# Kernel optimization log

Hardware: AMD Instinct MI355X
Metric: run time of the kernel (lower is better)

Reference implementation:

```python
import jax, jax.numpy as jnp
import numpy as np

SPARSITY = 0.9  # fraction of zeros in the weight matrix


def setup_inputs() -> dict:
    key = jax.random.key(0)
    k_x, k_w, k_m, k_b = jax.random.split(key, 4)
    in_features, out_features = 4096, 4096
    n_tokens = 8192
    x = jax.random.normal(k_x, (n_tokens, in_features), dtype=jnp.float32)
    weight = jax.random.normal(k_w, (out_features, in_features), dtype=jnp.float32)
    mask = jax.random.uniform(k_m, (out_features, in_features)) >= SPARSITY
    bias = jax.random.normal(k_b, (out_features,), dtype=jnp.float32)
    return {"x": x, "weight": weight, "mask": mask, "bias": bias}


def reference(x, weight, mask, bias):
    # SparseLinear.forward: batch_addmm(weight_sparse, x, bias) == x @ W^T + b
    # The sparse CSR/COO weight is represented here as (dense values * mask).
    w = jnp.where(mask, weight, jnp.zeros((), dtype=weight.dtype))
    return jnp.einsum('ni,oi->no', x, w) + bias
```

## Files before the change

kernel.cpp:

```cpp
#include <hip/hip_runtime.h>
#include <hip/hip_bf16.h>
#include <stdint.h>


#define MDIM 8192
#define NDIM 4096
#define KDIM 4096

typedef __bf16   bf16x8 __attribute__((ext_vector_type(8)));
typedef float    f32x4  __attribute__((ext_vector_type(4)));
typedef uint16_t u16x8  __attribute__((ext_vector_type(8)));

__device__ __forceinline__ uint16_t f32_to_bf16_rne(float f) {
  union { float f; uint32_t u; } v; v.f = f;
  uint32_t u = v.u;
  return (uint16_t)((u + 0x7fffu + ((u >> 16) & 1u)) >> 16);
}

__global__ void detect_mask_kernel(const uint32_t* __restrict__ mask,
                                   int* __restrict__ flag) {
  __shared__ int any_nonbool;
  if (threadIdx.x == 0) any_nonbool = 0;
  __syncthreads();
  int bad = 0;
  for (int i = threadIdx.x; i < 4096; i += 256) {
    uint32_t w = mask[i];
    bad |= (w > 1u) ? 1 : 0;
  }
  if (bad) any_nonbool = 1;
  __syncthreads();
  if (threadIdx.x == 0) *flag = any_nonbool;
}


__global__ void cvt_x_kernel(const float* __restrict__ x,
                             uint16_t* __restrict__ xh, int n8) {
  int i = blockIdx.x * blockDim.x + threadIdx.x;
  if (i >= n8) return;
  const float4* src = (const float4*)x + (size_t)i * 2;
  float4 a = src[0], b = src[1];
  u16x8 o;
  o[0] = f32_to_bf16_rne(a.x); o[1] = f32_to_bf16_rne(a.y);
  o[2] = f32_to_bf16_rne(a.z); o[3] = f32_to_bf16_rne(a.w);
  o[4] = f32_to_bf16_rne(b.x); o[5] = f32_to_bf16_rne(b.y);
  o[6] = f32_to_bf16_rne(b.z); o[7] = f32_to_bf16_rne(b.w);
  *((u16x8*)xh + i) = o;
}

__global__ void cvt_w_kernel(const float* __restrict__ w,
                             const void* __restrict__ mask,
                             const int* __restrict__ flag,
                             uint16_t* __restrict__ wh, int n8) {
  int i = blockIdx.x * blockDim.x + threadIdx.x;
  if (i >= n8) return;
  const float4* src = (const float4*)w + (size_t)i * 2;
  float4 a = src[0], b = src[1];
  float vals[8] = {a.x, a.y, a.z, a.w, b.x, b.y, b.z, b.w};
  int m[8];
  if (*flag) {
    uint64_t mb = *((const uint64_t*)mask + i);
#pragma unroll
    for (int j = 0; j < 8; ++j) m[j] = (int)((mb >> (8 * j)) & 0xffu);
  } else {
    const int4* mp = (const int4*)mask + (size_t)i * 2;
    int4 ma = mp[0], mb4 = mp[1];
    m[0] = ma.x; m[1] = ma.y; m[2] = ma.z; m[3] = ma.w;
    m[4] = mb4.x; m[5] = mb4.y; m[6] = mb4.z; m[7] = mb4.w;
  }
  u16x8 o;
#pragma unroll
  for (int j = 0; j < 8; ++j)
    o[j] = m[j] ? f32_to_bf16_rne(vals[j]) : (uint16_t)0;
  *((u16x8*)wh + i) = o;
}


__global__ __launch_bounds__(256) void gemm_bias_kernel(
    const uint16_t* __restrict__ A, const uint16_t* __restrict__ B,
    const float* __restrict__ bias, float* __restrict__ C) {
  constexpr int BM = 128, BN = 128, BK = 64;
  constexpr int NBN = NDIM / BN;
  constexpr int ROWB = BK * 2;

  __shared__ __align__(16) uint8_t smem[2 * BM * BK * 2];
  uint8_t* smA = smem;
  uint8_t* smB = smem + BM * BK * 2;

  const int bid = blockIdx.x;
  const int cpx = gridDim.x >> 3;
  const int wg  = (bid & 7) * cpx + (bid >> 3);
  const int bm  = wg / NBN;
  const int bn  = wg % NBN;

  const int tid  = threadIdx.x;
  const int wave = tid >> 6;
  const int lane = tid & 63;
  const int wm = wave >> 1, wn = wave & 1;
  const int fr = lane & 15;
  const int fq = lane >> 4;

  const int trow = tid >> 3;
  const int tcb  = (tid & 7) << 4;
  const int tcol = (tcb ^ ((trow & 7) << 4)) >> 1;

  const uint16_t* Ablk = A + (size_t)bm * BM * KDIM;
  const uint16_t* Bblk = B + (size_t)bn * BN * KDIM;

  const int swz = (lane & 7) << 4;
  const int rdA = (wm * 64 + fr) * ROWB;
  const int rdB = (wn * 64 + fr) * ROWB;
  const int cb0 = fq * 16;

  f32x4 acc[4][4] = {};

  for (int k0 = 0; k0 < KDIM; k0 += BK) {
#pragma unroll
    for (int is = 0; is < 4; ++is) {
      const uint16_t* src = Ablk + (size_t)(is * 32 + trow) * KDIM + (k0 + tcol);
      __builtin_amdgcn_global_load_lds(
          (const __attribute__((address_space(1))) void*)src,
          (__attribute__((address_space(3))) void*)(smA + is * 4096 + wave * 1024),
          16, 0, 0);
    }
#pragma unroll
    for (int is = 0; is < 4; ++is) {
      const uint16_t* src = Bblk + (size_t)(is * 32 + trow) * KDIM + (k0 + tcol);
      __builtin_amdgcn_global_load_lds(
          (const __attribute__((address_space(1))) void*)src,
          (__attribute__((address_space(3))) void*)(smB + is * 4096 + wave * 1024),
          16, 0, 0);
    }
    __syncthreads();

#pragma unroll
    for (int ks = 0; ks < 2; ++ks) {
      const int cb = cb0 + ks * 64;
      bf16x8 af[4], bfr[4];
#pragma unroll
      for (int mi = 0; mi < 4; ++mi)
        af[mi] = *(const bf16x8*)(smA + rdA + mi * 16 * ROWB + (cb ^ swz));
#pragma unroll
      for (int ni = 0; ni < 4; ++ni)
        bfr[ni] = *(const bf16x8*)(smB + rdB + ni * 16 * ROWB + (cb ^ swz));
#pragma unroll
      for (int mi = 0; mi < 4; ++mi)
#pragma unroll
        for (int ni = 0; ni < 4; ++ni)
          acc[mi][ni] = __builtin_amdgcn_mfma_f32_16x16x32_bf16(
              af[mi], bfr[ni], acc[mi][ni], 0, 0, 0);
    }
    __syncthreads();
  }

  const int rowg0 = bm * BM + wm * 64 + fq * 4;
  const int colg0 = bn * BN + wn * 64 + fr;
#pragma unroll
  for (int ni = 0; ni < 4; ++ni) {
    const int col = colg0 + ni * 16;
    const float bv = bias[col];
#pragma unroll
    for (int mi = 0; mi < 4; ++mi) {
#pragma unroll
      for (int j = 0; j < 4; ++j) {
        const int row = rowg0 + mi * 16 + j;
        C[(size_t)row * NDIM + col] = acc[mi][ni][j] + bv;
      }
    }
  }
}

extern "C" void kernel_launch(void* const* d_in, const int* in_sizes, int n_in,
                              void* d_out, int out_size, void* d_ws, size_t ws_size,
                              hipStream_t stream) {
  const float* x    = (const float*)d_in[0];
  const float* w    = (const float*)d_in[1];
  const void*  mk   = (const void*)d_in[2];
  const float* bias = (const float*)d_in[3];
  float* out        = (float*)d_out;

  const size_t need = (size_t)MDIM * KDIM * 2 + (size_t)NDIM * KDIM * 2;
  if (ws_size < need) return;

  uint16_t* xh = (uint16_t*)d_ws;
  uint16_t* wh = xh + (size_t)MDIM * KDIM;

  int* flag = (int*)d_out;
  detect_mask_kernel<<<1, 256, 0, stream>>>((const uint32_t*)mk, flag);

  const int nx8 = MDIM * KDIM / 8;
  const int nw8 = NDIM * KDIM / 8;
  cvt_x_kernel<<<nx8 / 256, 256, 0, stream>>>(x, xh, nx8);
  cvt_w_kernel<<<nw8 / 256, 256, 0, stream>>>(w, mk, flag, wh, nw8);

  const int grid = (MDIM / 128) * (NDIM / 128);
  gemm_bias_kernel<<<grid, 256, 0, stream>>>(xh, wh, bias, out);
}
```

Before: 680.3 us.

## Use 256x256 GEMM tiles with double-buffered async LDS loads and grid-stride converts

Moves the bf16 GEMM from 128x128 tiles with 4 waves to 256x256 tiles with 8 waves. Each wave now computes a 128x64 sub-tile, which raises data reuse per LDS byte. Global-to-LDS loads are double-buffered two tiles ahead, using partial vmcnt waits and raw barriers so loads overlap the MFMA work, and s_setprio is raised around the MFMA bursts. The conversion kernels switch to grid-stride loops with a fixed grid of 2048 blocks. The cost is more registers (128 accumulator floats per thread), 128 KB of LDS per block, and only 512 blocks in the grid, which may hurt occupancy or tail balance.

```diff
diff --git a/kernel.cpp b/kernel.cpp
--- a/kernel.cpp
+++ b/kernel.cpp
@@ -32,134 +32,164 @@
   if (threadIdx.x == 0) *flag = any_nonbool;
 }
 
-
 __global__ void cvt_x_kernel(const float* __restrict__ x,
                              uint16_t* __restrict__ xh, int n8) {
-  int i = blockIdx.x * blockDim.x + threadIdx.x;
-  if (i >= n8) return;
-  const float4* src = (const float4*)x + (size_t)i * 2;
-  float4 a = src[0], b = src[1];
-  u16x8 o;
-  o[0] = f32_to_bf16_rne(a.x); o[1] = f32_to_bf16_rne(a.y);
-  o[2] = f32_to_bf16_rne(a.z); o[3] = f32_to_bf16_rne(a.w);
-  o[4] = f32_to_bf16_rne(b.x); o[5] = f32_to_bf16_rne(b.y);
-  o[6] = f32_to_bf16_rne(b.z); o[7] = f32_to_bf16_rne(b.w);
-  *((u16x8*)xh + i) = o;
+  const int stride = gridDim.x * blockDim.x;
+  for (int i = blockIdx.x * blockDim.x + threadIdx.x; i < n8; i += stride) {
+    const float4* src = (const float4*)x + (size_t)i * 2;
+    float4 a = src[0], b = src[1];
+    u16x8 o;
+    o[0] = f32_to_bf16_rne(a.x); o[1] = f32_to_bf16_rne(a.y);
+    o[2] = f32_to_bf16_rne(a.z); o[3] = f32_to_bf16_rne(a.w);
+    o[4] = f32_to_bf16_rne(b.x); o[5] = f32_to_bf16_rne(b.y);
+    o[6] = f32_to_bf16_rne(b.z); o[7] = f32_to_bf16_rne(b.w);
+    *((u16x8*)xh + i) = o;
+  }
 }
 
 __global__ void cvt_w_kernel(const float* __restrict__ w,
                              const void* __restrict__ mask,
                              const int* __restrict__ flag,
                              uint16_t* __restrict__ wh, int n8) {
-  int i = blockIdx.x * blockDim.x + threadIdx.x;
-  if (i >= n8) return;
-  const float4* src = (const float4*)w + (size_t)i * 2;
-  float4 a = src[0], b = src[1];
-  float vals[8] = {a.x, a.y, a.z, a.w, b.x, b.y, b.z, b.w};
-  int m[8];
-  if (*flag) {
-    uint64_t mb = *((const uint64_t*)mask + i);
-#pragma unroll
-    for (int j = 0; j < 8; ++j) m[j] = (int)((mb >> (8 * j)) & 0xffu);
-  } else {
-    const int4* mp = (const int4*)mask + (size_t)i * 2;
-    int4 ma = mp[0], mb4 = mp[1];
-    m[0] = ma.x; m[1] = ma.y; m[2] = ma.z; m[3] = ma.w;
-    m[4] = mb4.x; m[5] = mb4.y; m[6] = mb4.z; m[7] = mb4.w;
-  }
-  u16x8 o;
-#pragma unroll
-  for (int j = 0; j < 8; ++j)
-    o[j] = m[j] ? f32_to_bf16_rne(vals[j]) : (uint16_t)0;
-  *((u16x8*)wh + i) = o;
-}
-
-
-__global__ __launch_bounds__(256) void gemm_bias_kernel(
+  const int stride = gridDim.x * blockDim.x;
+  const int isU8 = *flag;
+  for (int i = blockIdx.x * blockDim.x + threadIdx.x; i < n8; i += stride) {
+    const float4* src = (const float4*)w + (size_t)i * 2;
+    float4 a = src[0], b = src[1];
+    float vals[8] = {a.x, a.y, a.z, a.w, b.x, b.y, b.z, b.w};
+    int m[8];
+    if (isU8) {
+      uint64_t mb = *((const uint64_t*)mask + i);
+#pragma unroll
+      for (int j = 0; j < 8; ++j) m[j] = (int)((mb >> (8 * j)) & 0xffu);
+    } else {
+      const int4* mp = (const int4*)mask + (size_t)i * 2;
+      int4 ma = mp[0], mb4 = mp[1];
+      m[0] = ma.x; m[1] = ma.y; m[2] = ma.z; m[3] = ma.w;
+      m[4] = mb4.x; m[5] = mb4.y; m[6] = mb4.z; m[7] = mb4.w;
+    }
+    u16x8 o;
+#pragma unroll
+    for (int j = 0; j < 8; ++j)
+      o[j] = m[j] ? f32_to_bf16_rne(vals[j]) : (uint16_t)0;
+    *((u16x8*)wh + i) = o;
+  }
+}
+
+
+#define BARRIER() do { asm volatile("" ::: "memory");            \
+                       __builtin_amdgcn_s_barrier();             \
+                       asm volatile("" ::: "memory"); } while (0)
+#define WAITV8()  asm volatile("s_waitcnt vmcnt(8)" ::: "memory")
+#define WAITV0()  asm volatile("s_waitcnt vmcnt(0)" ::: "memory")
+
+__global__ __launch_bounds__(512, 2) void gemm_bias_256(
     const uint16_t* __restrict__ A, const uint16_t* __restrict__ B,
     const float* __restrict__ bias, float* __restrict__ C) {
-  constexpr int BM = 128, BN = 128, BK = 64;
+  constexpr int BM = 256, BN = 256, BK = 64;
+  constexpr int NT  = KDIM / BK;
   constexpr int NBN = NDIM / BN;
-  constexpr int ROWB = BK * 2;
-
-  __shared__ __align__(16) uint8_t smem[2 * BM * BK * 2];
-  uint8_t* smA = smem;
-  uint8_t* smB = smem + BM * BK * 2;
+
+  __shared__ __align__(16) uint8_t smem[2 * 65536];
 
   const int bid = blockIdx.x;
   const int cpx = gridDim.x >> 3;
   const int wg  = (bid & 7) * cpx + (bid >> 3);
-  const int bm  = wg / NBN;
-  const int bn  = wg % NBN;
+  const int bm  = wg / NBN, bn = wg % NBN;
 
   const int tid  = threadIdx.x;
-  const int wave = tid >> 6;
-  const int lane = tid & 63;
-  const int wm = wave >> 1, wn = wave & 1;
-  const int fr = lane & 15;
-  const int fq = lane >> 4;
+  const int wave = tid >> 6, lane = tid & 63;
+  const int wm = wave >> 2, wn = wave & 3;
+  const int fr = lane & 15, fq = lane >> 4;
 
   const int trow = tid >> 3;
   const int tcb  = (tid & 7) << 4;
   const int tcol = (tcb ^ ((trow & 7) << 4)) >> 1;
-
-  const uint16_t* Ablk = A + (size_t)bm * BM * KDIM;
-  const uint16_t* Bblk = B + (size_t)bn * BN * KDIM;
-
-  const int swz = (lane & 7) << 4;
-  const int rdA = (wm * 64 + fr) * ROWB;
-  const int rdB = (wn * 64 + fr) * ROWB;
-  const int cb0 = fq * 16;
-
-  f32x4 acc[4][4] = {};
-
-  for (int k0 = 0; k0 < KDIM; k0 += BK) {
-#pragma unroll
-    for (int is = 0; is < 4; ++is) {
-      const uint16_t* src = Ablk + (size_t)(is * 32 + trow) * KDIM + (k0 + tcol);
-      __builtin_amdgcn_global_load_lds(
-          (const __attribute__((address_space(1))) void*)src,
-          (__attribute__((address_space(3))) void*)(smA + is * 4096 + wave * 1024),
-          16, 0, 0);
+  const uint16_t* Ab = A + (size_t)bm * BM * KDIM;
+  const uint16_t* Bb = B + (size_t)bn * BN * KDIM;
+  const size_t aoff = (size_t)trow * KDIM + tcol;
+
+  const int c0 = ((fq) ^ (fr & 7)) << 4;
+  const int c1 = ((4 + fq) ^ (fr & 7)) << 4;
+
+  f32x4 acc[8][4] = {};
+
+#define STAGE(tile, bufbase) do {                                              \
+    const uint16_t* sa = Ab + (size_t)(tile) * BK + aoff;                      \
+    const uint16_t* sb = Bb + (size_t)(tile) * BK + aoff;                      \
+    _Pragma("unroll")                                                          \
+    for (int is = 0; is < 4; ++is) {                                           \
+      __builtin_amdgcn_global_load_lds(                                        \
+          (const __attribute__((address_space(1))) void*)(sa + (size_t)is * 64 * KDIM), \
+          (__attribute__((address_space(3))) void*)(smem + (bufbase) + is * 8192 + wave * 1024), \
+          16, 0, 0);                                                           \
+      __builtin_amdgcn_global_load_lds(                                        \
+          (const __attribute__((address_space(1))) void*)(sb + (size_t)is * 64 * KDIM), \
+          (__attribute__((address_space(3))) void*)(smem + (bufbase) + 32768 + is * 8192 + wave * 1024), \
+          16, 0, 0);                                                           \
+    }                                                                          \
+  } while (0)
+
+#define COMPUTE(bufbase) do {                                                  \
+    const uint8_t* bA = smem + (bufbase);                                      \
+    const uint8_t* bB = smem + (bufbase) + 32768;                              \
+    bf16x8 bfrag[4][2];                                                        \
+    _Pragma("unroll")                                                          \
+    for (int ni = 0; ni < 4; ++ni) {                                           \
+      const int brow = wn * 64 + ni * 16 + fr;                                 \
+      bfrag[ni][0] = *(const bf16x8*)(bB + brow * 128 + c0);                   \
+      bfrag[ni][1] = *(const bf16x8*)(bB + brow * 128 + c1);                   \
+    }                                                                          \
+    _Pragma("unroll")                                                          \
+    for (int mh = 0; mh < 2; ++mh) {                                           \
+      bf16x8 afrag[4][2];                                                      \
+      _Pragma("unroll")                                                        \
+      for (int mi = 0; mi < 4; ++mi) {                                         \
+        const int arow = wm * 128 + mh * 64 + mi * 16 + fr;                    \
+        afrag[mi][0] = *(const bf16x8*)(bA + arow * 128 + c0);                 \
+        afrag[mi][1] = *(const bf16x8*)(bA + arow * 128 + c1);                 \
+      }                                                                        \
+      __builtin_amdgcn_s_setprio(1);                                          \
+      _Pragma("unroll")                                                        \
+      for (int mi = 0; mi < 4; ++mi)                                           \
+        _Pragma("unroll")                                                      \
+        for (int ni = 0; ni < 4; ++ni) {                                       \
+          acc[mh * 4 + mi][ni] = __builtin_amdgcn_mfma_f32_16x16x32_bf16(      \
+              afrag[mi][0], bfrag[ni][0], acc[mh * 4 + mi][ni], 0, 0, 0);      \
+          acc[mh * 4 + mi][ni] = __builtin_amdgcn_mfma_f32_16x16x32_bf16(      \
+              afrag[mi][1], bfrag[ni][1], acc[mh * 4 + mi][ni], 0, 0, 0);      \
+        }                                                                      \
+      __builtin_amdgcn_s_setprio(0);                                          \
+    }                                                                          \
+  } while (0)
+
+  STAGE(0, 0);
+  STAGE(1, 65536);
+  WAITV8();
+  BARRIER();
+
+  for (int t = 0; t < NT; ++t) {
+    const uint32_t bo = (uint32_t)(t & 1) * 65536u;
+    COMPUTE(bo);
+    BARRIER();
+    if (t + 2 < NT) {
+      STAGE(t + 2, bo);
+      WAITV8();
+      BARRIER();
+    } else if (t + 1 < NT) {
+      WAITV0();
+      BARRIER();
     }
-#pragma unroll
-    for (int is = 0; is < 4; ++is) {
-      const uint16_t* src = Bblk + (size_t)(is * 32 + trow) * KDIM + (k0 + tcol);
-      __builtin_amdgcn_global_load_lds(
-          (const __attribute__((address_space(1))) void*)src,
-          (__attribute__((address_space(3))) void*)(smB + is * 4096 + wave * 1024),
-          16, 0, 0);
-    }
-    __syncthreads();
-
-#pragma unroll
-    for (int ks = 0; ks < 2; ++ks) {
-      const int cb = cb0 + ks * 64;
-      bf16x8 af[4], bfr[4];
-#pragma unroll
-      for (int mi = 0; mi < 4; ++mi)
-        af[mi] = *(const bf16x8*)(smA + rdA + mi * 16 * ROWB + (cb ^ swz));
-#pragma unroll
-      for (int ni = 0; ni < 4; ++ni)
-        bfr[ni] = *(const bf16x8*)(smB + rdB + ni * 16 * ROWB + (cb ^ swz));
-#pragma unroll
-      for (int mi = 0; mi < 4; ++mi)
-#pragma unroll
-        for (int ni = 0; ni < 4; ++ni)
-          acc[mi][ni] = __builtin_amdgcn_mfma_f32_16x16x32_bf16(
-              af[mi], bfr[ni], acc[mi][ni], 0, 0, 0);
-    }
-    __syncthreads();
-  }
-
-  const int rowg0 = bm * BM + wm * 64 + fq * 4;
+  }
+
+  const int rowg0 = bm * BM + wm * 128 + fq * 4;
   const int colg0 = bn * BN + wn * 64 + fr;
 #pragma unroll
   for (int ni = 0; ni < 4; ++ni) {
     const int col = colg0 + ni * 16;
     const float bv = bias[col];
 #pragma unroll
-    for (int mi = 0; mi < 4; ++mi) {
+    for (int mi = 0; mi < 8; ++mi) {
 #pragma unroll
       for (int j = 0; j < 4; ++j) {
         const int row = rowg0 + mi * 16 + j;
@@ -167,6 +197,8 @@
       }
     }
   }
+#undef STAGE
+#undef COMPUTE
 }
 
 extern "C" void kernel_launch(void* const* d_in, const int* in_sizes, int n_in,
@@ -189,9 +221,9 @@
 
   const int nx8 = MDIM * KDIM / 8;
   const int nw8 = NDIM * KDIM / 8;
-  cvt_x_kernel<<<nx8 / 256, 256, 0, stream>>>(x, xh, nx8);
-  cvt_w_kernel<<<nw8 / 256, 256, 0, stream>>>(w, mk, flag, wh, nw8);
-
-  const int grid = (MDIM / 128) * (NDIM / 128);
-  gemm_bias_kernel<<<grid, 256, 0, stream>>>(xh, wh, bias, out);
-}
+  cvt_x_kernel<<<2048, 256, 0, stream>>>(x, xh, nx8);
+  cvt_w_kernel<<<2048, 256, 0, stream>>>(w, mk, flag, wh, nw8);
+
+  const int grid = (MDIM / 256) * (NDIM / 256);
+  gemm_bias_256<<<grid, 512, 0, stream>>>(xh, wh, bias, out);
+}
```

After: 591.2 us. 13.1% less time.
